# Kernel tuning notes

Hardware: AMD Instinct MI355X
Metric: run time of the kernel (lower is better)

## Reference

```python
import jax, jax.numpy as jnp
import numpy as np

GROUP = 128  # quantization group size along the input dimension


def dequant(q, scales, zeros):
    # q: [out, in] int4 codes stored as int32 in [0,16)
    # scales, zeros: [out, in//GROUP] per-group affine params
    out_dim, in_dim = q.shape
    g = in_dim // GROUP
    w = (q.astype(jnp.float32).reshape(out_dim, g, GROUP) - zeros[:, :, None]) * scales[:, :, None]
    return w.reshape(out_dim, in_dim)


def setup_inputs() -> dict:
    key = jax.random.key(0)
    ks = jax.random.split(key, 10)
    H, I = 4096, 11008
    B, S = 64, 1
    inp = {
        "x": jax.random.normal(ks[0], (B, S, H), dtype=jnp.float32),
        "gate_qweight": jax.random.randint(ks[1], (I, H), 0, 16, dtype=jnp.int32),
        "gate_scales": jax.random.uniform(ks[2], (I, H // GROUP), dtype=jnp.float32) * 0.02,
        "gate_zeros": jax.random.uniform(ks[3], (I, H // GROUP), dtype=jnp.float32) * 16.0,
        "up_qweight": jax.random.randint(ks[4], (I, H), 0, 16, dtype=jnp.int32),
        "up_scales": jax.random.uniform(ks[5], (I, H // GROUP), dtype=jnp.float32) * 0.02,
        "up_zeros": jax.random.uniform(ks[6], (I, H // GROUP), dtype=jnp.float32) * 16.0,
        "down_qweight": jax.random.randint(ks[7], (H, I), 0, 16, dtype=jnp.int32),
        "down_scales": jax.random.uniform(ks[8], (H, I // GROUP), dtype=jnp.float32) * 0.02,
        "down_zeros": jax.random.uniform(ks[9], (H, I // GROUP), dtype=jnp.float32) * 16.0,
    }
    return inp


def reference(x, gate_qweight, gate_scales, gate_zeros,
              up_qweight, up_scales, up_zeros,
              down_qweight, down_scales, down_zeros):
    Wg = dequant(gate_qweight, gate_scales, gate_zeros)   # [I, H]
    Wu = dequant(up_qweight, up_scales, up_zeros)         # [I, H]
    Wd = dequant(down_qweight, down_scales, down_zeros)   # [H, I]
    gate = jnp.einsum('bsh,ih->bsi', x, Wg)
    up = jnp.einsum('bsh,ih->bsi', x, Wu)
    h = jax.nn.silu(gate) * up                             # SwiGLU
    return jnp.einsum('bsi,hi->bsh', h, Wd)
```

## Files before the change

kernel.cpp:

```cpp
#include <hip/hip_runtime.h>
#include <hip/hip_bf16.h>
#include <stdint.h>

#define H_DIM 4096
#define I_DIM 11008
#define NGH   32
#define NGI   86
#define KWH   512
#define KWI   1376
#define NWV   5636096

typedef __attribute__((ext_vector_type(8))) short short8;
typedef __attribute__((ext_vector_type(4))) short s16x4;
typedef __attribute__((ext_vector_type(4))) float f32x4;
typedef __attribute__((ext_vector_type(4))) int   i32x4;

static __device__ __forceinline__ short f2bf(float f) {
  union { __hip_bfloat16 b; short s; } u;
  u.b = __float2bfloat16(f);
  return u.s;
}

static __device__ __forceinline__ void pack_tile(
    char* smem, const int* __restrict__ src, int RL, int KW,
    int* __restrict__ dstM, int tile)
{
  unsigned short (*sb)[72] = (unsigned short(*)[72])smem;
  int rt, ct;
  if (RL == H_DIM) { rt = tile >> 4; ct = tile & 15; }
  else             { rt = tile / 43; ct = tile - rt * 43; }
  const int t = threadIdx.x & 255;
  const int rowl = t >> 4, j = t & 15;
  const int* rp = src + (size_t)(rt * 16 + rowl) * RL + ct * 256;
#pragma unroll
  for (int p = 0; p < 4; ++p) {
    i32x4 v = *(const i32x4*)(rp + p * 64 + j * 4);
    sb[rowl][p * 16 + j] = (unsigned short)((v[0] & 15) | ((v[1] & 15) << 4)
                        | ((v[2] & 15) << 8) | ((v[3] & 15) << 12));
  }
  __syncthreads();
  int* dst = dstM + ((size_t)rt * KW + ct * 32) * 16;
#pragma unroll
  for (int p = 0; p < 2; ++p) {
    const int wi = t + p * 256;
    const int kwl = wi >> 4, ri = wi & 15;
    dst[wi] = (int)sb[ri][2 * kwl] | ((int)sb[ri][2 * kwl + 1] << 16);
  }
}

template<int UP>
static __device__ __forceinline__ void gemm_gu_body(
    char* smem, const short* __restrict__ xb, const int* __restrict__ pktM,
    const float* __restrict__ sc, const float* __restrict__ ze,
    float* __restrict__ gsum, short* __restrict__ hb)
{
  float (*red)[4][4][64] = (float(*)[4][4][64])smem;
  const int rt   = blockIdx.x;
  const int n0   = rt * 16;
  const int w    = threadIdx.x >> 6;
  const int l    = threadIdx.x & 63;
  const int col  = l & 15;
  const int krow = l >> 4;
  const int i    = n0 + col;

  const int* B = pktM + (size_t)rt * (KWH * 16) + col;

  float sv[4], zv[4];
#pragma unroll
  for (int g = 0; g < 4; ++g) {
    const int gg = w * 4 + g;
    sv[g] = sc[(size_t)i * NGH + gg];
    zv[g] = ze[(size_t)i * NGH + gg] * sv[g];
  }

  f32x4 acc[4];
#pragma unroll
  for (int c = 0; c < 4; ++c)
#pragma unroll
    for (int r = 0; r < 4; ++r) acc[c][r] = 0.f;

  const int wb  = w * 64;
  const int ks0 = w * 512 + krow * 8;

  int qA = B[(wb + krow) * 16], qB;
  short8 aA[4], aB[4];
#pragma unroll
  for (int c = 0; c < 4; ++c)
    aA[c] = *(const short8*)(xb + (size_t)(c * 16 + col) * H_DIM + ks0);

#pragma unroll
  for (int u = 0; u < 8; ++u) {
    const int t1 = 2 * u + 1;
    const int t2 = (2 * u + 2) & 15;
    const int g  = u >> 1;
    qB = B[(wb + 4 * t1 + krow) * 16];
#pragma unroll
    for (int c = 0; c < 4; ++c)
      aB[c] = *(const short8*)(xb + (size_t)(c * 16 + col) * H_DIM + ks0 + t1 * 32);
    {
      short8 b;
#pragma unroll
      for (int j = 0; j < 8; ++j)
        b[j] = f2bf((float)((qA >> (4 * j)) & 15) * sv[g] - zv[g]);
#pragma unroll
      for (int c = 0; c < 4; ++c)
        acc[c] = __builtin_amdgcn_mfma_f32_16x16x32_bf16(aA[c], b, acc[c], 0, 0, 0);
    }
    qA = B[(wb + 4 * t2 + krow) * 16];
#pragma unroll
    for (int c = 0; c < 4; ++c)
      aA[c] = *(const short8*)(xb + (size_t)(c * 16 + col) * H_DIM + ks0 + t2 * 32);
    {
      short8 b;
#pragma unroll
      for (int j = 0; j < 8; ++j)
        b[j] = f2bf((float)((qB >> (4 * j)) & 15) * sv[g] - zv[g]);
#pragma unroll
      for (int c = 0; c < 4; ++c)
        acc[c] = __builtin_amdgcn_mfma_f32_16x16x32_bf16(aB[c], b, acc[c], 0, 0, 0);
    }
  }

#pragma unroll
  for (int c = 0; c < 4; ++c)
#pragma unroll
    for (int r = 0; r < 4; ++r)
      red[w][c][r][l] = acc[c][r];
  __syncthreads();

  const int c2 = threadIdx.x >> 7;
  const int rh = (threadIdx.x >> 6) & 1;
  const int ll = threadIdx.x & 63;
#pragma unroll
  for (int rr = 0; rr < 2; ++rr) {
    const int r = rh * 2 + rr;
    float s = 0.f;
#pragma unroll
    for (int ww = 0; ww < 8; ++ww) s += red[ww][c2][r][ll];
    const int m  = c2 * 16 + (ll >> 4) * 4 + r;
    const int ii = n0 + (ll & 15);
    if (UP) {
      const float gv = gsum[(size_t)m * I_DIM + ii];
      const float hv = gv / (1.f + __expf(-gv)) * s;
      hb[(size_t)m * I_DIM + ii] = f2bf(hv);
    } else {
      gsum[(size_t)m * I_DIM + ii] = s;
    }
  }
}

__global__ __launch_bounds__(512, 4) void packG_xcvt_kernel(
    const float* __restrict__ x, short* __restrict__ xb,
    const int* __restrict__ gq, int* __restrict__ gp)
{
  __shared__ char smem[4608];
  if (blockIdx.x < 128) {
    const int i = (blockIdx.x * 512 + threadIdx.x) * 4;
    f32x4 v = *(const f32x4*)(x + i);
    s16x4 o;
    o[0] = f2bf(v[0]); o[1] = f2bf(v[1]); o[2] = f2bf(v[2]); o[3] = f2bf(v[3]);
    *(s16x4*)(xb + i) = o;
    return;
  }
  const int pb = blockIdx.x - 128;
  const int half = threadIdx.x >> 8;
  pack_tile(smem + half * 2304, gq, H_DIM, KWH, gp, pb * 2 + half);
}

__global__ __launch_bounds__(512, 4) void gateU_kernel(
    const short* __restrict__ xb, const int* __restrict__ gp,
    const float* __restrict__ gsc, const float* __restrict__ gze,
    float* __restrict__ gsum, const int* __restrict__ uq, int* __restrict__ upk)
{
  __shared__ char smem[32768];
  if (blockIdx.x < 688) {
    gemm_gu_body<0>(smem, xb, gp, gsc, gze, gsum, nullptr);
    return;
  }
  const int pb = blockIdx.x - 688;
  const int half = threadIdx.x >> 8;
  pack_tile(smem + half * 2304, uq, H_DIM, KWH, upk, pb * 2 + half);
}

__global__ __launch_bounds__(512, 4) void upD_kernel(
    const short* __restrict__ xb, const int* __restrict__ upk,
    const float* __restrict__ usc, const float* __restrict__ uze,
    float* __restrict__ gsum, short* __restrict__ hb,
    const int* __restrict__ dq, int* __restrict__ dpk)
{
  __shared__ char smem[32768];
  if (blockIdx.x < 688) {
    gemm_gu_body<1>(smem, xb, upk, usc, uze, gsum, hb);
    return;
  }
  const int pb = blockIdx.x - 688;
  const int half = threadIdx.x >> 8;
  pack_tile(smem + half * 2304, dq, I_DIM, KWI, dpk, pb * 2 + half);
}

__global__ __launch_bounds__(512, 4) void phase2p_kernel(
    const short* __restrict__ hb, const int* __restrict__ dpt,
    const float* __restrict__ dsc, const float* __restrict__ dze,
    float* __restrict__ part)
{
  __shared__ float red[8][4][4][64];
  const int tile  = blockIdx.x & 255;
  const int split = blockIdx.x >> 8;
  const int n0   = tile * 16;
  const int w    = threadIdx.x >> 6;
  const int l    = threadIdx.x & 63;
  const int col  = l & 15;
  const int krow = l >> 4;
  const int n    = n0 + col;

  const int* dB = dpt + (size_t)tile * (KWI * 16) + col;

  f32x4 acc[4];
#pragma unroll
  for (int c = 0; c < 4; ++c)
#pragma unroll
    for (int r = 0; r < 4; ++r) acc[c][r] = 0.f;

  const int cnt    = (w < 6) ? 11 : 10;
  const int sstart = (w < 6) ? w * 11 : 66 + (w - 6) * 10;
  const int kbase  = split * 2752 + sstart * 32;
  const int wbase  = split * 344 + sstart * 4;

  const int g0 = kbase >> 7;
  float s0 = dsc[(size_t)n * NGI + g0];
  float s1 = dsc[(size_t)n * NGI + min(g0 + 1, NGI - 1)];
  float s2 = dsc[(size_t)n * NGI + min(g0 + 2, NGI - 1)];
  float s3 = dsc[(size_t)n * NGI + min(g0 + 3, NGI - 1)];
  float z0 = dze[(size_t)n * NGI + g0] * s0;
  float z1 = dze[(size_t)n * NGI + min(g0 + 1, NGI - 1)] * s1;
  float z2 = dze[(size_t)n * NGI + min(g0 + 2, NGI - 1)] * s2;
  float z3 = dze[(size_t)n * NGI + min(g0 + 3, NGI - 1)] * s3;

  int qdA = dB[(wbase + krow) * 16], qdB_;
  short8 aA[4], aB[4];
#pragma unroll
  for (int c = 0; c < 4; ++c)
    aA[c] = *(const short8*)(hb + (size_t)(c * 16 + col) * I_DIM + kbase + krow * 8);

  const int nh = cnt >> 1;
#pragma unroll 1
  for (int u = 0; u < nh; ++u) {
    const int t0 = 2 * u, t1 = 2 * u + 1;
    const int t2 = (t1 + 1 < cnt) ? (t1 + 1) : 0;
    qdB_ = dB[(wbase + 4 * t1 + krow) * 16];
#pragma unroll
    for (int c = 0; c < 4; ++c)
      aB[c] = *(const short8*)(hb + (size_t)(c * 16 + col) * I_DIM + kbase + t1 * 32 + krow * 8);
    {
      const int gi = ((kbase + t0 * 32) >> 7) - g0;
      const float sv = gi == 0 ? s0 : gi == 1 ? s1 : gi == 2 ? s2 : s3;
      const float zv = gi == 0 ? z0 : gi == 1 ? z1 : gi == 2 ? z2 : z3;
      short8 b;
#pragma unroll
      for (int j = 0; j < 8; ++j)
        b[j] = f2bf((float)((qdA >> (4 * j)) & 15) * sv - zv);
#pragma unroll
      for (int c = 0; c < 4; ++c)
        acc[c] = __builtin_amdgcn_mfma_f32_16x16x32_bf16(aA[c], b, acc[c], 0, 0, 0);
    }
    qdA = dB[(wbase + 4 * t2 + krow) * 16];
#pragma unroll
    for (int c = 0; c < 4; ++c)
      aA[c] = *(const short8*)(hb + (size_t)(c * 16 + col) * I_DIM + kbase + t2 * 32 + krow * 8);
    {
      const int gi = ((kbase + t1 * 32) >> 7) - g0;
      const float sv = gi == 0 ? s0 : gi == 1 ? s1 : gi == 2 ? s2 : s3;
      const float zv = gi == 0 ? z0 : gi == 1 ? z1 : gi == 2 ? z2 : z3;
      short8 b;
#pragma unroll
      for (int j = 0; j < 8; ++j)
        b[j] = f2bf((float)((qdB_ >> (4 * j)) & 15) * sv - zv);
#pragma unroll
      for (int c = 0; c < 4; ++c)
        acc[c] = __builtin_amdgcn_mfma_f32_16x16x32_bf16(aB[c], b, acc[c], 0, 0, 0);
    }
  }
  if (cnt & 1) {
    const int t0 = cnt - 1;
    const int gi = ((kbase + t0 * 32) >> 7) - g0;
    const float sv = gi == 0 ? s0 : gi == 1 ? s1 : gi == 2 ? s2 : s3;
    const float zv = gi == 0 ? z0 : gi == 1 ? z1 : gi == 2 ? z2 : z3;
    short8 b;
#pragma unroll
    for (int j = 0; j < 8; ++j)
      b[j] = f2bf((float)((qdA >> (4 * j)) & 15) * sv - zv);
#pragma unroll
    for (int c = 0; c < 4; ++c)
      acc[c] = __builtin_amdgcn_mfma_f32_16x16x32_bf16(aA[c], b, acc[c], 0, 0, 0);
  }

#pragma unroll
  for (int c = 0; c < 4; ++c)
#pragma unroll
    for (int r = 0; r < 4; ++r)
      red[w][c][r][l] = acc[c][r];
  __syncthreads();

  if (threadIdx.x < 256) {
    const int c2 = threadIdx.x >> 6;
    const int ll = threadIdx.x & 63;
    float* po = part + (size_t)split * (64 * H_DIM);
#pragma unroll
    for (int r = 0; r < 4; ++r) {
      float s = 0.f;
#pragma unroll
      for (int ww = 0; ww < 8; ++ww) s += red[ww][c2][r][ll];
      const int m  = c2 * 16 + (ll >> 4) * 4 + r;
      const int nn = n0 + (ll & 15);
      po[(size_t)m * H_DIM + nn] = s;
    }
  }
}

__global__ void reduce4_kernel(const float* __restrict__ part, float* __restrict__ out) {
  const int idx = (blockIdx.x * 256 + threadIdx.x) * 4;
  const int S = 64 * H_DIM;
  f32x4 s0 = *(const f32x4*)(part + idx);
  f32x4 s1 = *(const f32x4*)(part + S + idx);
  f32x4 s2 = *(const f32x4*)(part + 2 * S + idx);
  f32x4 s3 = *(const f32x4*)(part + 3 * S + idx);
  f32x4 r = (s0 + s1) + (s2 + s3);
  *(f32x4*)(out + idx) = r;
}

__global__ void xcvt_kernel(const float* __restrict__ x, short* __restrict__ xb) {
  int i = (blockIdx.x * 256 + threadIdx.x) * 4;
  f32x4 v = *(const f32x4*)(x + i);
  s16x4 o;
  o[0] = f2bf(v[0]); o[1] = f2bf(v[1]); o[2] = f2bf(v[2]); o[3] = f2bf(v[3]);
  *(s16x4*)(xb + i) = o;
}

__global__ __launch_bounds__(512, 4) void phase1f_kernel(
    const short* __restrict__ xb,
    const int* __restrict__ gq, const float* __restrict__ gsc, const float* __restrict__ gze,
    const int* __restrict__ uq, const float* __restrict__ usc, const float* __restrict__ uze,
    short* __restrict__ hb)
{
  __shared__ float red[8][4][4][64];
  const int n0   = blockIdx.x * 16;
  const int w    = threadIdx.x >> 6;
  const int l    = threadIdx.x & 63;
  const int col  = l & 15;
  const int krow = l >> 4;
  const int i    = n0 + col;
  const int*   gqr = gq + (size_t)i * H_DIM;
  const int*   uqr = uq + (size_t)i * H_DIM;
  const float* gsr = gsc + (size_t)i * NGH;
  const float* gzr = gze + (size_t)i * NGH;
  const float* usr = usc + (size_t)i * NGH;
  const float* uzr = uze + (size_t)i * NGH;
  f32x4 accG[4], accU[4];
#pragma unroll
  for (int c = 0; c < 4; ++c)
#pragma unroll
    for (int r = 0; r < 4; ++r) { accG[c][r] = 0.f; accU[c][r] = 0.f; }
  const int kw = w * 512;
#pragma unroll 1
  for (int g = 0; g < 4; ++g) {
    const int gg = w * 4 + g;
    const float sg = gsr[gg], zg = gzr[gg] * sg;
    const float su = usr[gg], zu = uzr[gg] * su;
#pragma unroll
    for (int ks = 0; ks < 4; ++ks) {
      const int koff = kw + g * 128 + ks * 32 + krow * 8;
      i32x4 q0 = *(const i32x4*)(gqr + koff);
      i32x4 q1 = *(const i32x4*)(gqr + koff + 4);
      i32x4 p0 = *(const i32x4*)(uqr + koff);
      i32x4 p1 = *(const i32x4*)(uqr + koff + 4);
      short8 a[4];
#pragma unroll
      for (int c = 0; c < 4; ++c)
        a[c] = *(const short8*)(xb + (size_t)(c * 16 + col) * H_DIM + koff);
      short8 bg, bu;
#pragma unroll
      for (int j = 0; j < 4; ++j) {
        bg[j]     = f2bf((float)q0[j] * sg - zg);
        bg[j + 4] = f2bf((float)q1[j] * sg - zg);
        bu[j]     = f2bf((float)p0[j] * su - zu);
        bu[j + 4] = f2bf((float)p1[j] * su - zu);
      }
#pragma unroll
      for (int c = 0; c < 4; ++c) {
        accG[c] = __builtin_amdgcn_mfma_f32_16x16x32_bf16(a[c], bg, accG[c], 0, 0, 0);
        accU[c] = __builtin_amdgcn_mfma_f32_16x16x32_bf16(a[c], bu, accU[c], 0, 0, 0);
      }
    }
  }
  const int c2 = threadIdx.x >> 7;
  const int rh = (threadIdx.x >> 6) & 1;
  const int ll = threadIdx.x & 63;
#pragma unroll
  for (int c = 0; c < 4; ++c)
#pragma unroll
    for (int r = 0; r < 4; ++r)
      red[w][c][r][l] = accG[c][r];
  __syncthreads();
  float gsum[2];
#pragma unroll
  for (int rr = 0; rr < 2; ++rr) {
    const int r = rh * 2 + rr;
    float s = 0.f;
#pragma unroll
    for (int ww = 0; ww < 8; ++ww) s += red[ww][c2][r][ll];
    gsum[rr] = s;
  }
  __syncthreads();
#pragma unroll
  for (int c = 0; c < 4; ++c)
#pragma unroll
    for (int r = 0; r < 4; ++r)
      red[w][c][r][l] = accU[c][r];
  __syncthreads();
#pragma unroll
  for (int rr = 0; rr < 2; ++rr) {
    const int r = rh * 2 + rr;
    float us = 0.f;
#pragma unroll
    for (int ww = 0; ww < 8; ++ww) us += red[ww][c2][r][ll];
    const float gv = gsum[rr];
    const float hv = gv / (1.f + __expf(-gv)) * us;
    const int m  = c2 * 16 + (ll >> 4) * 4 + r;
    const int ii = n0 + (ll & 15);
    hb[(size_t)m * I_DIM + ii] = f2bf(hv);
  }
}

__global__ __launch_bounds__(512, 4) void phase2f_kernel(
    const short* __restrict__ hb,
    const int* __restrict__ dq, const float* __restrict__ dsc, const float* __restrict__ dze,
    float* __restrict__ part)
{
  __shared__ float red[8][4][4][64];
  const int tile  = blockIdx.x & 255;
  const int split = blockIdx.x >> 8;
  const int n0   = tile * 16;
  const int w    = threadIdx.x >> 6;
  const int l    = threadIdx.x & 63;
  const int col  = l & 15;
  const int krow = l >> 4;
  const int n    = n0 + col;
  const int*   dqr = dq + (size_t)n * I_DIM;
  const float* dsr = dsc + (size_t)n * NGI;
  const float* dzr = dze + (size_t)n * NGI;
  f32x4 acc[4];
#pragma unroll
  for (int c = 0; c < 4; ++c)
#pragma unroll
    for (int r = 0; r < 4; ++r) acc[c][r] = 0.f;
  const int cnt    = (w < 6) ? 11 : 10;
  const int sstart = (w < 6) ? w * 11 : 66 + (w - 6) * 10;
  const int kbase  = split * 2752 + sstart * 32;
  int gprev = -1;
  float sv = 0.f, zv = 0.f;
#pragma unroll 1
  for (int s = 0; s < cnt; ++s) {
    const int k0 = kbase + s * 32;
    const int g  = k0 >> 7;
    if (g != gprev) { sv = dsr[g]; zv = dzr[g] * sv; gprev = g; }
    i32x4 q0 = *(const i32x4*)(dqr + k0 + krow * 8);
    i32x4 q1 = *(const i32x4*)(dqr + k0 + krow * 8 + 4);
    short8 a[4];
#pragma unroll
    for (int c = 0; c < 4; ++c)
      a[c] = *(const short8*)(hb + (size_t)(c * 16 + col) * I_DIM + k0 + krow * 8);
    short8 b;
#pragma unroll
    for (int j = 0; j < 4; ++j) {
      b[j]     = f2bf((float)q0[j] * sv - zv);
      b[j + 4] = f2bf((float)q1[j] * sv - zv);
    }
#pragma unroll
    for (int c = 0; c < 4; ++c)
      acc[c] = __builtin_amdgcn_mfma_f32_16x16x32_bf16(a[c], b, acc[c], 0, 0, 0);
  }
#pragma unroll
  for (int c = 0; c < 4; ++c)
#pragma unroll
    for (int r = 0; r < 4; ++r)
      red[w][c][r][l] = acc[c][r];
  __syncthreads();
  if (threadIdx.x < 256) {
    const int c2 = threadIdx.x >> 6;
    const int ll = threadIdx.x & 63;
    float* po = part + (size_t)split * (64 * H_DIM);
#pragma unroll
    for (int r = 0; r < 4; ++r) {
      float s = 0.f;
#pragma unroll
      for (int ww = 0; ww < 8; ++ww) s += red[ww][c2][r][ll];
      const int m  = c2 * 16 + (ll >> 4) * 4 + r;
      const int nn = n0 + (ll & 15);
      po[(size_t)m * H_DIM + nn] = s;
    }
  }
}

extern "C" void kernel_launch(void* const* d_in, const int* in_sizes, int n_in,
                              void* d_out, int out_size, void* d_ws, size_t ws_size,
                              hipStream_t stream) {
  const float* x  = (const float*)d_in[0];
  const int*   gq = (const int*)d_in[1];
  const float* gs = (const float*)d_in[2];
  const float* gz = (const float*)d_in[3];
  const int*   uq = (const int*)d_in[4];
  const float* us = (const float*)d_in[5];
  const float* uz = (const float*)d_in[6];
  const int*   dq = (const int*)d_in[7];
  const float* ds = (const float*)d_in[8];
  const float* dz = (const float*)d_in[9];
  float* out = (float*)d_out;

  const size_t XB   = (size_t)64 * H_DIM * 2;
  const size_t HB   = (size_t)64 * I_DIM * 2;
  const size_t PART = (size_t)4 * 64 * H_DIM * 4;
  const size_t PK   = (size_t)NWV * 4;

  short* xb   = (short*)d_ws;
  short* hb   = (short*)((char*)d_ws + XB);
  float* part = (float*)((char*)d_ws + XB + HB);
  int*   pkt  = (int*)((char*)d_ws + XB + HB + PART);
  int*   gp   = pkt;
  int*   upk  = pkt + (size_t)NWV;
  int*   dpk  = pkt + 2 * (size_t)NWV;

  if (ws_size >= XB + HB + PART + 3 * PK) {
    packG_xcvt_kernel<<<128 + 5504, 512, 0, stream>>>(x, xb, gq, gp);
    gateU_kernel<<<688 + 5504, 512, 0, stream>>>(xb, gp, gs, gz, part, uq, upk);
    upD_kernel<<<688 + 5504, 512, 0, stream>>>(xb, upk, us, uz, part, hb, dq, dpk);
    phase2p_kernel<<<(H_DIM / 16) * 4, 512, 0, stream>>>(hb, dpk, ds, dz, part);
  } else {
    xcvt_kernel<<<(64 * H_DIM) / 1024, 256, 0, stream>>>(x, xb);
    phase1f_kernel<<<I_DIM / 16, 512, 0, stream>>>(xb, gq, gs, gz, uq, us, uz, hb);
    phase2f_kernel<<<(H_DIM / 16) * 4, 512, 0, stream>>>(hb, dq, ds, dz, part);
  }
  reduce4_kernel<<<(64 * H_DIM) / 1024, 256, 0, stream>>>(part, out);
}
```

Before: 219.3 us.

## Compute two 16-column weight tiles per gate/up GEMM block to reuse activations

Each gate/up GEMM block now covers 32 output columns (two packed weight tiles) instead of 16. Every activation fragment loaded from xb feeds eight MFMAs instead of four, which halves activation traffic per output and halves the number of GEMM blocks. The pack blocks are interleaved into the odd indices of the first 688 slots, keeping the fused grid layout. The cost is higher register pressure from doubled accumulators and scale values, plus a second reduction pass through shared memory with an extra barrier.

```diff
diff --git a/kernel.cpp b/kernel.cpp
--- a/kernel.cpp
+++ b/kernel.cpp
@@ -52,37 +52,43 @@
 static __device__ __forceinline__ void gemm_gu_body(
     char* smem, const short* __restrict__ xb, const int* __restrict__ pktM,
     const float* __restrict__ sc, const float* __restrict__ ze,
-    float* __restrict__ gsum, short* __restrict__ hb)
+    float* __restrict__ gsum, short* __restrict__ hb, int rtb)
 {
   float (*red)[4][4][64] = (float(*)[4][4][64])smem;
-  const int rt   = blockIdx.x;
-  const int n0   = rt * 16;
+  const int n0   = rtb * 32;
   const int w    = threadIdx.x >> 6;
   const int l    = threadIdx.x & 63;
   const int col  = l & 15;
   const int krow = l >> 4;
-  const int i    = n0 + col;
-
-  const int* B = pktM + (size_t)rt * (KWH * 16) + col;
-
-  float sv[4], zv[4];
-#pragma unroll
-  for (int g = 0; g < 4; ++g) {
-    const int gg = w * 4 + g;
-    sv[g] = sc[(size_t)i * NGH + gg];
-    zv[g] = ze[(size_t)i * NGH + gg] * sv[g];
-  }
-
-  f32x4 acc[4];
-#pragma unroll
-  for (int c = 0; c < 4; ++c)
-#pragma unroll
-    for (int r = 0; r < 4; ++r) acc[c][r] = 0.f;
+
+  const int* B0 = pktM + (size_t)(2 * rtb)     * (KWH * 16) + col;
+  const int* B1 = pktM + (size_t)(2 * rtb + 1) * (KWH * 16) + col;
+
+  float sv[2][4], zv[2][4];
+#pragma unroll
+  for (int cg = 0; cg < 2; ++cg) {
+    const int i = n0 + cg * 16 + col;
+#pragma unroll
+    for (int g = 0; g < 4; ++g) {
+      const int gg = w * 4 + g;
+      sv[cg][g] = sc[(size_t)i * NGH + gg];
+      zv[cg][g] = ze[(size_t)i * NGH + gg] * sv[cg][g];
+    }
+  }
+
+  f32x4 acc[2][4];
+#pragma unroll
+  for (int cg = 0; cg < 2; ++cg)
+#pragma unroll
+    for (int c = 0; c < 4; ++c)
+#pragma unroll
+      for (int r = 0; r < 4; ++r) acc[cg][c][r] = 0.f;
 
   const int wb  = w * 64;
   const int ks0 = w * 512 + krow * 8;
 
-  int qA = B[(wb + krow) * 16], qB;
+  int q0A = B0[(wb + krow) * 16], q1A = B1[(wb + krow) * 16];
+  int q0B, q1B;
   short8 aA[4], aB[4];
 #pragma unroll
   for (int c = 0; c < 4; ++c)
@@ -93,59 +99,72 @@
     const int t1 = 2 * u + 1;
     const int t2 = (2 * u + 2) & 15;
     const int g  = u >> 1;
-    qB = B[(wb + 4 * t1 + krow) * 16];
+    q0B = B0[(wb + 4 * t1 + krow) * 16];
+    q1B = B1[(wb + 4 * t1 + krow) * 16];
 #pragma unroll
     for (int c = 0; c < 4; ++c)
       aB[c] = *(const short8*)(xb + (size_t)(c * 16 + col) * H_DIM + ks0 + t1 * 32);
     {
-      short8 b;
-#pragma unroll
-      for (int j = 0; j < 8; ++j)
-        b[j] = f2bf((float)((qA >> (4 * j)) & 15) * sv[g] - zv[g]);
-#pragma unroll
-      for (int c = 0; c < 4; ++c)
-        acc[c] = __builtin_amdgcn_mfma_f32_16x16x32_bf16(aA[c], b, acc[c], 0, 0, 0);
-    }
-    qA = B[(wb + 4 * t2 + krow) * 16];
+      short8 b0, b1;
+#pragma unroll
+      for (int j = 0; j < 8; ++j) {
+        b0[j] = f2bf((float)((q0A >> (4 * j)) & 15) * sv[0][g] - zv[0][g]);
+        b1[j] = f2bf((float)((q1A >> (4 * j)) & 15) * sv[1][g] - zv[1][g]);
+      }
+#pragma unroll
+      for (int c = 0; c < 4; ++c) {
+        acc[0][c] = __builtin_amdgcn_mfma_f32_16x16x32_bf16(aA[c], b0, acc[0][c], 0, 0, 0);
+        acc[1][c] = __builtin_amdgcn_mfma_f32_16x16x32_bf16(aA[c], b1, acc[1][c], 0, 0, 0);
+      }
+    }
+    q0A = B0[(wb + 4 * t2 + krow) * 16];
+    q1A = B1[(wb + 4 * t2 + krow) * 16];
 #pragma unroll
     for (int c = 0; c < 4; ++c)
       aA[c] = *(const short8*)(xb + (size_t)(c * 16 + col) * H_DIM + ks0 + t2 * 32);
     {
-      short8 b;
-#pragma unroll
-      for (int j = 0; j < 8; ++j)
-        b[j] = f2bf((float)((qB >> (4 * j)) & 15) * sv[g] - zv[g]);
-#pragma unroll
-      for (int c = 0; c < 4; ++c)
-        acc[c] = __builtin_amdgcn_mfma_f32_16x16x32_bf16(aB[c], b, acc[c], 0, 0, 0);
-    }
-  }
-
-#pragma unroll
-  for (int c = 0; c < 4; ++c)
-#pragma unroll
-    for (int r = 0; r < 4; ++r)
-      red[w][c][r][l] = acc[c][r];
-  __syncthreads();
+      short8 b0, b1;
+#pragma unroll
+      for (int j = 0; j < 8; ++j) {
+        b0[j] = f2bf((float)((q0B >> (4 * j)) & 15) * sv[0][g] - zv[0][g]);
+        b1[j] = f2bf((float)((q1B >> (4 * j)) & 15) * sv[1][g] - zv[1][g]);
+      }
+#pragma unroll
+      for (int c = 0; c < 4; ++c) {
+        acc[0][c] = __builtin_amdgcn_mfma_f32_16x16x32_bf16(aB[c], b0, acc[0][c], 0, 0, 0);
+        acc[1][c] = __builtin_amdgcn_mfma_f32_16x16x32_bf16(aB[c], b1, acc[1][c], 0, 0, 0);
+      }
+    }
+  }
 
   const int c2 = threadIdx.x >> 7;
   const int rh = (threadIdx.x >> 6) & 1;
   const int ll = threadIdx.x & 63;
 #pragma unroll
-  for (int rr = 0; rr < 2; ++rr) {
-    const int r = rh * 2 + rr;
-    float s = 0.f;
-#pragma unroll
-    for (int ww = 0; ww < 8; ++ww) s += red[ww][c2][r][ll];
-    const int m  = c2 * 16 + (ll >> 4) * 4 + r;
-    const int ii = n0 + (ll & 15);
-    if (UP) {
-      const float gv = gsum[(size_t)m * I_DIM + ii];
-      const float hv = gv / (1.f + __expf(-gv)) * s;
-      hb[(size_t)m * I_DIM + ii] = f2bf(hv);
-    } else {
-      gsum[(size_t)m * I_DIM + ii] = s;
-    }
+  for (int cg = 0; cg < 2; ++cg) {
+#pragma unroll
+    for (int c = 0; c < 4; ++c)
+#pragma unroll
+      for (int r = 0; r < 4; ++r)
+        red[w][c][r][l] = acc[cg][c][r];
+    __syncthreads();
+#pragma unroll
+    for (int rr = 0; rr < 2; ++rr) {
+      const int r = rh * 2 + rr;
+      float s = 0.f;
+#pragma unroll
+      for (int ww = 0; ww < 8; ++ww) s += red[ww][c2][r][ll];
+      const int m  = c2 * 16 + (ll >> 4) * 4 + r;
+      const int ii = n0 + cg * 16 + (ll & 15);
+      if (UP) {
+        const float gv = gsum[(size_t)m * I_DIM + ii];
+        const float hv = gv / (1.f + __expf(-gv)) * s;
+        hb[(size_t)m * I_DIM + ii] = f2bf(hv);
+      } else {
+        gsum[(size_t)m * I_DIM + ii] = s;
+      }
+    }
+    if (cg == 0) __syncthreads();
   }
 }
 
@@ -173,11 +192,12 @@
     float* __restrict__ gsum, const int* __restrict__ uq, int* __restrict__ upk)
 {
   __shared__ char smem[32768];
-  if (blockIdx.x < 688) {
-    gemm_gu_body<0>(smem, xb, gp, gsc, gze, gsum, nullptr);
+  const int j = blockIdx.x;
+  if (j < 688 && (j & 1) == 0) {
+    gemm_gu_body<0>(smem, xb, gp, gsc, gze, gsum, nullptr, j >> 1);
     return;
   }
-  const int pb = blockIdx.x - 688;
+  const int pb = (j < 688) ? (j >> 1) : (j - 344);
   const int half = threadIdx.x >> 8;
   pack_tile(smem + half * 2304, uq, H_DIM, KWH, upk, pb * 2 + half);
 }
@@ -189,11 +209,12 @@
     const int* __restrict__ dq, int* __restrict__ dpk)
 {
   __shared__ char smem[32768];
-  if (blockIdx.x < 688) {
-    gemm_gu_body<1>(smem, xb, upk, usc, uze, gsum, hb);
+  const int j = blockIdx.x;
+  if (j < 688 && (j & 1) == 0) {
+    gemm_gu_body<1>(smem, xb, upk, usc, uze, gsum, hb, j >> 1);
     return;
   }
-  const int pb = blockIdx.x - 688;
+  const int pb = (j < 688) ? (j >> 1) : (j - 344);
   const int half = threadIdx.x >> 8;
   pack_tile(smem + half * 2304, dq, I_DIM, KWI, dpk, pb * 2 + half);
 }
@@ -531,8 +552,8 @@
 
   if (ws_size >= XB + HB + PART + 3 * PK) {
     packG_xcvt_kernel<<<128 + 5504, 512, 0, stream>>>(x, xb, gq, gp);
-    gateU_kernel<<<688 + 5504, 512, 0, stream>>>(xb, gp, gs, gz, part, uq, upk);
-    upD_kernel<<<688 + 5504, 512, 0, stream>>>(xb, upk, us, uz, part, hb, dq, dpk);
+    gateU_kernel<<<344 + 5504, 512, 0, stream>>>(xb, gp, gs, gz, part, uq, upk);
+    upD_kernel<<<344 + 5504, 512, 0, stream>>>(xb, upk, us, uz, part, hb, dq, dpk);
     phase2p_kernel<<<(H_DIM / 16) * 4, 512, 0, stream>>>(hb, dpk, ds, dz, part);
   } else {
     xcvt_kernel<<<(64 * H_DIM) / 1024, 256, 0, stream>>>(x, xb);
```

New measurement: 221.3 us. About the same (+0.9%).
